# Kernel optimization log

Measured on AMD Instinct MI355X. Metric: run time of the kernel, lower is better.

Reference implementation:

```python
import jax, jax.numpy as jnp
import numpy as np

N_USERS = 50000
N_ENTITIES = 100000
N_FACTORS = 8
N_RELATIONS = 17  # weight has n_relations-1 = 16 rows
EMB = 64
N_EDGES = 2_000_000
NNZ = 2_000_000
SLOPE = 0.2


def setup_inputs() -> dict:
    key = jax.random.key(0)
    ks = jax.random.split(key, 16)
    inp = {
        "entity_emb": jax.random.normal(ks[0], (N_ENTITIES, EMB), jnp.float32),
        "user_emb": jax.random.normal(ks[1], (N_USERS, EMB), jnp.float32),
        "latent_emb": jax.random.normal(ks[2], (N_FACTORS, EMB), jnp.float32),
        "edge_index": jax.random.randint(ks[3], (2, N_EDGES), 0, N_ENTITIES, jnp.int32),
        "edge_type": jax.random.randint(ks[4], (N_EDGES,), 1, N_RELATIONS, jnp.int32),
        "interact_rows": jax.random.randint(ks[5], (NNZ,), 0, N_USERS, jnp.int32),
        "interact_cols": jax.random.randint(ks[6], (NNZ,), 0, N_ENTITIES, jnp.int32),
        "interact_vals": jax.random.uniform(ks[7], (NNZ,), jnp.float32),
        "weight": jax.random.normal(ks[8], (N_RELATIONS - 1, EMB), jnp.float32),
        "entity_cate_set": jax.random.randint(ks[9], (N_ENTITIES,), 1, 33, jnp.int32),
        # params (torch Linear convention: y = x @ W.T + b)
        "W_user_att": jax.random.normal(ks[10], (N_FACTORS, N_FACTORS), jnp.float32) * 0.1,
        "b_user_att": jnp.zeros((N_FACTORS,), jnp.float32),
        "W_weight_att": jax.random.normal(ks[11], (N_RELATIONS - 1, N_RELATIONS - 1), jnp.float32) * 0.1,
        "b_weight_att": jnp.zeros((N_RELATIONS - 1,), jnp.float32),
        "W1": jax.random.normal(ks[12], (EMB, EMB), jnp.float32) * 0.1,
        "b1": jnp.zeros((EMB,), jnp.float32),
        "W2": jax.random.normal(ks[13], (EMB, EMB), jnp.float32) * 0.1,
        "b2": jnp.zeros((EMB,), jnp.float32),
    }
    return inp


def _lin(x, W, b):
    return x @ W.T + b


def reference(entity_emb, user_emb, latent_emb, edge_index, edge_type,
              interact_rows, interact_cols, interact_vals, weight, entity_cate_set,
              W_user_att, b_user_att, W_weight_att, b_weight_att, W1, b1, W2, b2):
    head, tail = edge_index[0], edge_index[1]

    # KG aggregate: gather-multiply-scatter_mean (is_div=False branch)
    neigh = entity_emb[tail] * weight[edge_type - 1]            # [E, C]
    sums = jax.ops.segment_sum(neigh, head, num_segments=N_ENTITIES)
    cnt = jax.ops.segment_sum(jnp.ones((neigh.shape[0],), neigh.dtype),
                              head, num_segments=N_ENTITIES)
    entity_agg = sums / jnp.maximum(cnt, 1.0)[:, None]          # [N_ent, C]

    # user aggregate: sparse mm (COO) interact_mat @ entity_emb
    user_agg = jax.ops.segment_sum(interact_vals[:, None] * entity_emb[interact_cols],
                                   interact_rows, num_segments=N_USERS)  # [U, C]

    # user -> latent interest attention
    score_ = _lin(user_emb, W1, b1) @ _lin(latent_emb, W1, b1).T          # [U, F]
    score = jax.nn.softmax(jax.nn.leaky_relu(_lin(score_, W_user_att, b_user_att), SLOPE), axis=1)  # [U, F]

    score_rp = _lin(latent_emb, W2, b2) @ _lin(weight, W2, b2).T          # [F, R-1]
    latent_new = jax.nn.softmax(jax.nn.leaky_relu(_lin(score_rp, W_weight_att, b_weight_att), SLOPE), axis=-1) @ weight  # [F, C]

    # (disen_weight * score).sum(dim=1) == score @ latent_new
    user_agg = user_agg * (score @ latent_new) + user_agg
    return (entity_agg, user_agg, latent_new)
```

## Files before the change

### kernel.cpp

```cpp
#include <hip/hip_runtime.h>

#define N_USERS    50000
#define N_ENTITIES 100000
#define EMB        64
#define N_EDGES    2000000
#define NNZ        2000000
#define SLOPE      0.2f

#define KROWS   64
#define KSHIFT  6
#define NBK     1563
#define UROWS   32
#define USHIFT  5
#define NBU     1563
#define CAPK    2048
#define CAPU    2048
#define KCAP    1536
#define UCAP    1536
#define CHK     8192
#define EPT     (CHK / 512)
#define PB_K    ((N_EDGES + CHK - 1) / CHK)
#define PB_U    ((NNZ + CHK - 1) / CHK)
#define NQ      (NBK + NBU)
#define ACCBLK  512

__global__ __launch_bounds__(512) void init_cur(int* __restrict__ kgCur,
                                                int* __restrict__ uCur,
                                                int* __restrict__ qCtr) {
    int t = blockIdx.x * blockDim.x + threadIdx.x;
    if (t < NBK) kgCur[t] = t * KCAP;
    if (t < NBU) uCur[t]  = t * UCAP;
    if (t == 0) qCtr[0] = 0;
}

__device__ void small_dense_body(int l,
                                 const float* __restrict__ latent_emb,
                                 const float* __restrict__ weight,
                                 const float* __restrict__ W_weight_att,
                                 const float* __restrict__ b_weight_att,
                                 const float* __restrict__ W1,
                                 const float* __restrict__ b1,
                                 const float* __restrict__ W2,
                                 const float* __restrict__ b2,
                                 float* __restrict__ P_out,
                                 float* __restrict__ c_out,
                                 float* __restrict__ latent_new_out) {
    __shared__ float lat1[8 * 64];
    __shared__ float lat2[8 * 64];
    __shared__ float wl2[16 * 64];
    __shared__ float srp[8 * 16];
    __shared__ float soft[8 * 16];

    if (l < 64) {
        for (int f = 0; f < 8; ++f) {
            float a1 = b1[l], a2 = b2[l];
            for (int k = 0; k < 64; ++k) {
                float le = latent_emb[f * 64 + k];
                a1 += le * W1[l * 64 + k];
                a2 += le * W2[l * 64 + k];
            }
            lat1[f * 64 + l] = a1;
            lat2[f * 64 + l] = a2;
        }
        for (int r = 0; r < 16; ++r) {
            float a = b2[l];
            for (int k = 0; k < 64; ++k) a += weight[r * 64 + k] * W2[l * 64 + k];
            wl2[r * 64 + l] = a;
        }
    }
    __syncthreads();

    if (l < 64) {
        for (int f = 0; f < 8; ++f) {
            float p = 0.f;
            for (int d = 0; d < 64; ++d) p += W1[d * 64 + l] * lat1[f * 64 + d];
            P_out[l * 8 + f] = p;
        }
        if (l < 8) {
            float cc = 0.f;
            for (int d = 0; d < 64; ++d) cc += b1[d] * lat1[l * 64 + d];
            c_out[l] = cc;
        }
        for (int idx = l; idx < 128; idx += 64) {
            int f = idx >> 4, r = idx & 15;
            float a = 0.f;
            for (int d = 0; d < 64; ++d) a += lat2[f * 64 + d] * wl2[r * 64 + d];
            srp[idx] = a;
        }
    }
    __syncthreads();

    if (l < 8) {
        int f = l;
        float att[16];
        float mx = -1e30f;
        for (int k = 0; k < 16; ++k) {
            float a = b_weight_att[k];
            for (int j = 0; j < 16; ++j) a += srp[f * 16 + j] * W_weight_att[k * 16 + j];
            a = a > 0.f ? a : SLOPE * a;
            att[k] = a;
            mx = fmaxf(mx, a);
        }
        float s = 0.f;
        for (int k = 0; k < 16; ++k) { att[k] = expf(att[k] - mx); s += att[k]; }
        float inv = 1.f / s;
        for (int k = 0; k < 16; ++k) soft[f * 16 + k] = att[k] * inv;
    }
    __syncthreads();

    if (l < 64) {
        for (int f = 0; f < 8; ++f) {
            float a = 0.f;
            for (int r = 0; r < 16; ++r) a += soft[f * 16 + r] * weight[r * 64 + l];
            latent_new_out[f * 64 + l] = a;
        }
    }
}

__global__ void small_dense(const float* __restrict__ latent_emb,
                            const float* __restrict__ weight,
                            const float* __restrict__ W_weight_att,
                            const float* __restrict__ b_weight_att,
                            const float* __restrict__ W1,
                            const float* __restrict__ b1,
                            const float* __restrict__ W2,
                            const float* __restrict__ b2,
                            float* __restrict__ P_out,
                            float* __restrict__ c_out,
                            float* __restrict__ latent_new_out) {
    small_dense_body(threadIdx.x, latent_emb, weight, W_weight_att, b_weight_att,
                     W1, b1, W2, b2, P_out, c_out, latent_new_out);
}

__global__ __launch_bounds__(512) void scatter_both(const int* __restrict__ head,
                                                    const int* __restrict__ tail,
                                                    const int* __restrict__ etype,
                                                    int* __restrict__ kgCur,
                                                    int* __restrict__ kgPay,
                                                    const int* __restrict__ urows,
                                                    const int* __restrict__ ucols,
                                                    const float* __restrict__ uvals,
                                                    int* __restrict__ uCur,
                                                    int2* __restrict__ uPay,
                                                    const float* __restrict__ latent_emb,
                                                    const float* __restrict__ weight,
                                                    const float* __restrict__ W_weight_att,
                                                    const float* __restrict__ b_weight_att,
                                                    const float* __restrict__ W1,
                                                    const float* __restrict__ b1,
                                                    const float* __restrict__ W2,
                                                    const float* __restrict__ b2,
                                                    float* __restrict__ Pbuf,
                                                    float* __restrict__ cbuf,
                                                    float* __restrict__ lat_out) {
    if (blockIdx.x == PB_K + PB_U) {
        small_dense_body(threadIdx.x, latent_emb, weight, W_weight_att,
                         b_weight_att, W1, b1, W2, b2, Pbuf, cbuf, lat_out);
        return;
    }

    __shared__ int lh[NBK];
    __shared__ int lb[NBK];
    int tid = threadIdx.x;
    bool isKg = blockIdx.x < PB_K;
    int base = (isKg ? blockIdx.x : blockIdx.x - PB_K) * CHK;
    int shift = isKg ? KSHIFT : USHIFT;
    const int* src = isKg ? head : urows;
    int* cur = isKg ? kgCur : uCur;

    for (int t = tid; t < NBK; t += 512) lh[t] = 0;
    __syncthreads();

    int hreg[EPT];
#pragma unroll
    for (int j = 0; j < EPT; ++j) {
        int i = base + j * 512 + tid;
        int h = (i < N_EDGES) ? src[i] : -1;
        hreg[j] = h;
        if (h >= 0) atomicAdd(&lh[h >> shift], 1);
    }
    __syncthreads();
    for (int t = tid; t < NBK; t += 512) {
        int c = lh[t];
        lb[t] = c ? atomicAdd(&cur[t], c) : 0;
        lh[t] = 0;
    }
    __syncthreads();
    if (isKg) {
#pragma unroll
        for (int j = 0; j < EPT; ++j) {
            int h = hreg[j];
            if (h >= 0) {
                int i = base + j * 512 + tid;
                int b = h >> KSHIFT;
                int p = lb[b] + atomicAdd(&lh[b], 1);
                kgPay[p] = tail[i] | ((etype[i] - 1) << 17) | ((h & (KROWS - 1)) << 21);
            }
        }
    } else {
#pragma unroll
        for (int j = 0; j < EPT; ++j) {
            int h = hreg[j];
            if (h >= 0) {
                int i = base + j * 512 + tid;
                int b = h >> USHIFT;
                int p = lb[b] + atomicAdd(&lh[b], 1);
                uPay[p] = make_int2(ucols[i] | ((h & (UROWS - 1)) << 17),
                                    __float_as_int(uvals[i]));
            }
        }
    }
}

__global__ __launch_bounds__(1024, 8) void acc_both(
        const int* __restrict__ kgPay, const int* __restrict__ kgCur,
        const int2* __restrict__ uPay, const int* __restrict__ uCur,
        const float* __restrict__ entity_emb,
        const float* __restrict__ weight,
        const float* __restrict__ user_emb,
        const float* __restrict__ P,
        const float* __restrict__ cvec,
        const float* __restrict__ W_user_att,
        const float* __restrict__ b_user_att,
        const float* __restrict__ latent_new,
        int* __restrict__ qCtr,
        float* __restrict__ ent_out,
        float* __restrict__ user_out) {
    __shared__ long long smem8[2097];
    __shared__ int sbk;
    int t = threadIdx.x, d = t & 63, wv = t >> 6;

    for (;;) {
        __syncthreads();
        if (t == 0) sbk = atomicAdd(qCtr, 1);
        __syncthreads();
        int q = sbk;
        if (q >= NQ) return;

        if (q < NBU) {
            int2* spay = (int2*)smem8;
            int* lcnt = (int*)(spay + CAPU);
            int* lofs = lcnt + UROWS;
            int* sc   = lofs + UROWS + 1;
            int bk = q;
            int start = bk * UCAP, end = uCur[bk];
            int n = end - start; if (n > CAPU) n = CAPU;

            if (t < UROWS) lcnt[t] = 0;
            __syncthreads();
            for (int i = t; i < n; i += 1024)
                atomicAdd(&lcnt[(uPay[start + i].x >> 17) & (UROWS - 1)], 1);
            __syncthreads();
            if (t < UROWS) sc[t] = lcnt[t];
            __syncthreads();
            for (int off = 1; off < UROWS; off <<= 1) {
                int v = (t < UROWS && t >= off) ? sc[t - off] : 0;
                __syncthreads();
                if (t < UROWS) sc[t] += v;
                __syncthreads();
            }
            if (t < UROWS) { int e = sc[t] - lcnt[t]; lofs[t] = e; lcnt[t] = e; }
            if (t == 0) lofs[UROWS] = n;
            __syncthreads();
            for (int i = t; i < n; i += 1024) {
                int2 v = uPay[start + i];
                int p = atomicAdd(&lcnt[(v.x >> 17) & (UROWS - 1)], 1);
                spay[p] = v;
            }
            __syncthreads();

            int rowbase = bk * UROWS;
            for (int rr = 0; rr < UROWS / 16; ++rr) {
                int r = wv * (UROWS / 16) + rr;
                int gr = rowbase + r;
                if (gr >= N_USERS) break;
                int s0 = lofs[r], e0 = lofs[r + 1];
                float acc = 0.f;
                int i = s0;
                for (; i + 7 < e0; i += 8) {
                    float a0 = 0.f, a1 = 0.f;
#pragma unroll
                    for (int u = 0; u < 8; u += 2) {
                        int2 va = spay[i + u], vb = spay[i + u + 1];
                        a0 += __int_as_float(va.y) * entity_emb[(va.x & 0x1FFFF) * EMB + d];
                        a1 += __int_as_float(vb.y) * entity_emb[(vb.x & 0x1FFFF) * EMB + d];
                    }
                    acc += a0 + a1;
                }
                for (; i < e0; ++i) {
                    int2 v = spay[i];
                    acc += __int_as_float(v.y) * entity_emb[(v.x & 0x1FFFF) * EMB + d];
                }
                for (int j = start + CAPU; j < end; ++j) {
                    int2 v = uPay[j];
                    if (((v.x >> 17) & (UROWS - 1)) == r)
                        acc += __int_as_float(v.y) * entity_emb[(v.x & 0x1FFFF) * EMB + d];
                }

                float ue = user_emb[gr * EMB + d];
                float s[8];
#pragma unroll
                for (int f = 0; f < 8; ++f) s[f] = ue * P[d * 8 + f];
#pragma unroll
                for (int off = 32; off; off >>= 1) {
#pragma unroll
                    for (int f = 0; f < 8; ++f) s[f] += __shfl_xor(s[f], off, 64);
                }
#pragma unroll
                for (int f = 0; f < 8; ++f) s[f] += cvec[f];
                float att[8];
                float mx = -1e30f;
#pragma unroll
                for (int k = 0; k < 8; ++k) {
                    float a = b_user_att[k];
#pragma unroll
                    for (int j = 0; j < 8; ++j) a += s[j] * W_user_att[k * 8 + j];
                    a = a > 0.f ? a : SLOPE * a;
                    att[k] = a;
                    mx = fmaxf(mx, a);
                }
                float sum = 0.f;
#pragma unroll
                for (int k = 0; k < 8; ++k) { att[k] = __expf(att[k] - mx); sum += att[k]; }
                float inv = 1.f / sum;
                float g = 0.f;
#pragma unroll
                for (int f = 0; f < 8; ++f) g += att[f] * inv * latent_new[f * EMB + d];
                user_out[gr * EMB + d] = acc * (1.f + g);
            }
        } else {
            int* spay = (int*)smem8;
            int* lcnt = spay + CAPK;
            int* lofs = lcnt + KROWS;
            int* sc   = lofs + KROWS + 1;
            int bk = q - NBU;
            int start = bk * KCAP, end = kgCur[bk];
            int n = end - start; if (n > CAPK) n = CAPK;

            if (t < KROWS) lcnt[t] = 0;
            __syncthreads();
            for (int i = t; i < n; i += 1024)
                atomicAdd(&lcnt[(kgPay[start + i] >> 21) & (KROWS - 1)], 1);
            __syncthreads();
            if (t < KROWS) sc[t] = lcnt[t];
            __syncthreads();
            for (int off = 1; off < KROWS; off <<= 1) {
                int v = (t < KROWS && t >= off) ? sc[t - off] : 0;
                __syncthreads();
                if (t < KROWS) sc[t] += v;
                __syncthreads();
            }
            if (t < KROWS) { int e = sc[t] - lcnt[t]; lofs[t] = e; lcnt[t] = e; }
            if (t == 0) lofs[KROWS] = n;
            __syncthreads();
            for (int i = t; i < n; i += 1024) {
                int v = kgPay[start + i];
                int p = atomicAdd(&lcnt[(v >> 21) & (KROWS - 1)], 1);
                spay[p] = v;
            }
            __syncthreads();

            int rowbase = bk * KROWS;
            for (int rr = 0; rr < KROWS / 16; ++rr) {
                int r = wv * (KROWS / 16) + rr;
                int gr = rowbase + r;
                if (gr >= N_ENTITIES) break;
                int s0 = lofs[r], e0 = lofs[r + 1];
                int cnt = e0 - s0;
                float acc = 0.f;
                int i = s0;
                for (; i + 7 < e0; i += 8) {
                    float a0 = 0.f, a1 = 0.f;
#pragma unroll
                    for (int u = 0; u < 8; u += 2) {
                        int va = spay[i + u], vb = spay[i + u + 1];
                        a0 += entity_emb[(va & 0x1FFFF) * EMB + d] * weight[((va >> 17) & 15) * EMB + d];
                        a1 += entity_emb[(vb & 0x1FFFF) * EMB + d] * weight[((vb >> 17) & 15) * EMB + d];
                    }
                    acc += a0 + a1;
                }
                for (; i < e0; ++i) {
                    int v = spay[i];
                    acc += entity_emb[(v & 0x1FFFF) * EMB + d] * weight[((v >> 17) & 15) * EMB + d];
                }
                for (int j = start + CAPK; j < end; ++j) {
                    int v = kgPay[j];
                    if (((v >> 21) & (KROWS - 1)) == r) {
                        acc += entity_emb[(v & 0x1FFFF) * EMB + d] * weight[((v >> 17) & 15) * EMB + d];
                        ++cnt;
                    }
                }
                ent_out[gr * EMB + d] = acc / fmaxf((float)cnt, 1.f);
            }
        }
    }
}

__global__ void kg_scatter(const int* __restrict__ head, const int* __restrict__ tail,
                           const int* __restrict__ etype,
                           const float* __restrict__ entity_emb,
                           const float* __restrict__ weight,
                           float* __restrict__ sums, float* __restrict__ cnt) {
    int gid = blockIdx.x * blockDim.x + threadIdx.x;
    int e = gid >> 6, d = threadIdx.x & 63;
    if (e >= N_EDGES) return;
    int h = head[e], t = tail[e], w = etype[e] - 1;
    float v = entity_emb[t * EMB + d] * weight[w * EMB + d];
    unsafeAtomicAdd(&sums[h * EMB + d], v);
    if (d == 0) unsafeAtomicAdd(&cnt[h], 1.0f);
}

__global__ void user_scatter(const int* __restrict__ rows, const int* __restrict__ cols,
                             const float* __restrict__ vals,
                             const float* __restrict__ entity_emb,
                             float* __restrict__ user_sums) {
    int gid = blockIdx.x * blockDim.x + threadIdx.x;
    int e = gid >> 6, d = threadIdx.x & 63;
    if (e >= NNZ) return;
    float v = vals[e] * entity_emb[cols[e] * EMB + d];
    unsafeAtomicAdd(&user_sums[rows[e] * EMB + d], v);
}

__global__ void entity_div(float* __restrict__ ent, const float* __restrict__ cnt) {
    int gid = blockIdx.x * blockDim.x + threadIdx.x;
    if (gid >= N_ENTITIES * EMB) return;
    float c = cnt[gid >> 6];
    ent[gid] = ent[gid] / fmaxf(c, 1.0f);
}

__global__ void user_finalize(const float* __restrict__ user_emb,
                              const float* __restrict__ P,
                              const float* __restrict__ c,
                              const float* __restrict__ W_user_att,
                              const float* __restrict__ b_user_att,
                              const float* __restrict__ latent_new,
                              float* __restrict__ user_out) {
    int gid = blockIdx.x * blockDim.x + threadIdx.x;
    int u = gid >> 6, lane = threadIdx.x & 63;
    if (u >= N_USERS) return;
    float ue = user_emb[u * 64 + lane];
    float s[8];
#pragma unroll
    for (int f = 0; f < 8; ++f) s[f] = ue * P[lane * 8 + f];
#pragma unroll
    for (int off = 32; off; off >>= 1)
#pragma unroll
        for (int f = 0; f < 8; ++f) s[f] += __shfl_xor(s[f], off, 64);
#pragma unroll
    for (int f = 0; f < 8; ++f) s[f] += c[f];
    float att[8], mx = -1e30f;
#pragma unroll
    for (int k = 0; k < 8; ++k) {
        float a = b_user_att[k];
#pragma unroll
        for (int j = 0; j < 8; ++j) a += s[j] * W_user_att[k * 8 + j];
        a = a > 0.f ? a : SLOPE * a;
        att[k] = a;
        mx = fmaxf(mx, a);
    }
    float sum = 0.f;
#pragma unroll
    for (int k = 0; k < 8; ++k) { att[k] = expf(att[k] - mx); sum += att[k]; }
    float inv = 1.f / sum, g = 0.f;
#pragma unroll
    for (int f = 0; f < 8; ++f) g += att[f] * inv * latent_new[f * 64 + lane];
    float ua = user_out[u * 64 + lane];
    user_out[u * 64 + lane] = ua * (1.f + g);
}

extern "C" void kernel_launch(void* const* d_in, const int* in_sizes, int n_in,
                              void* d_out, int out_size, void* d_ws, size_t ws_size,
                              hipStream_t stream) {
    const float* entity_emb   = (const float*)d_in[0];
    const float* user_emb     = (const float*)d_in[1];
    const float* latent_emb   = (const float*)d_in[2];
    const int*   edge_index   = (const int*)d_in[3];
    const int*   edge_type    = (const int*)d_in[4];
    const int*   irows        = (const int*)d_in[5];
    const int*   icols        = (const int*)d_in[6];
    const float* ivals        = (const float*)d_in[7];
    const float* weight       = (const float*)d_in[8];
    const float* W_user_att   = (const float*)d_in[10];
    const float* b_user_att   = (const float*)d_in[11];
    const float* W_weight_att = (const float*)d_in[12];
    const float* b_weight_att = (const float*)d_in[13];
    const float* W1           = (const float*)d_in[14];
    const float* b1           = (const float*)d_in[15];
    const float* W2           = (const float*)d_in[16];
    const float* b2           = (const float*)d_in[17];

    float* out      = (float*)d_out;
    float* ent_out  = out;
    float* user_out = out + (size_t)N_ENTITIES * EMB;
    float* lat_out  = user_out + (size_t)N_USERS * EMB;

    const int* head = edge_index;
    const int* tail = edge_index + N_EDGES;

    int* ws_i = (int*)d_ws;
    int*   qCtr   = ws_i;
    int*   kgCur  = qCtr + 2;
    int*   uCur   = kgCur + NBK;
    int*   kgPay  = uCur + NBU;
    int2*  uPay   = (int2*)(kgPay + NBK * KCAP);
    float* Pbuf   = (float*)(uPay + NBU * UCAP);
    float* cbuf   = Pbuf + 64 * 8;
    size_t need_static = (size_t)(2 + NBK + NBU + (size_t)NBK * KCAP +
                                  2 * (size_t)NBU * UCAP + 512 + 8) * 4;

    if (ws_size >= need_static) {
        init_cur<<<(NBK + 511) / 512, 512, 0, stream>>>(kgCur, uCur, qCtr);
        scatter_both<<<PB_K + PB_U + 1, 512, 0, stream>>>(head, tail, edge_type,
                                                          kgCur, kgPay,
                                                          irows, icols, ivals,
                                                          uCur, uPay,
                                                          latent_emb, weight,
                                                          W_weight_att, b_weight_att,
                                                          W1, b1, W2, b2,
                                                          Pbuf, cbuf, lat_out);
        acc_both<<<ACCBLK, 1024, 0, stream>>>(kgPay, kgCur, uPay, uCur,
                                              entity_emb, weight, user_emb,
                                              Pbuf, cbuf, W_user_att, b_user_att,
                                              lat_out, qCtr, ent_out, user_out);
    } else {
        float* cnt   = (float*)d_ws;
        float* Pbuf3 = cnt + N_ENTITIES;
        float* cbuf3 = Pbuf3 + 64 * 8;
        hipMemsetAsync(ent_out, 0,
                       (size_t)(N_ENTITIES + N_USERS) * EMB * sizeof(float), stream);
        hipMemsetAsync(cnt, 0, N_ENTITIES * sizeof(float), stream);
        int blocks_edges = (N_EDGES * 64) / 256;
        kg_scatter<<<blocks_edges, 256, 0, stream>>>(head, tail, edge_type, entity_emb,
                                                     weight, ent_out, cnt);
        user_scatter<<<blocks_edges, 256, 0, stream>>>(irows, icols, ivals, entity_emb,
                                                       user_out);
        small_dense<<<1, 64, 0, stream>>>(latent_emb, weight, W_weight_att,
                                          b_weight_att, W1, b1, W2, b2,
                                          Pbuf3, cbuf3, lat_out);
        user_finalize<<<(N_USERS * 64) / 256, 256, 0, stream>>>(user_emb, Pbuf3, cbuf3,
                                                                W_user_att, b_user_att,
                                                                lat_out, user_out);
        entity_div<<<(N_ENTITIES * EMB) / 256, 256, 0, stream>>>(ent_out, cnt);
    }
}
```

Baseline: 398.3 us.

## Fuse bucket scatter and accumulation into one persistent kernel with grid barrier

Merges the cursor init, the bucket-scatter pass and the accumulate pass into one persistent kernel. Blocks pull scatter chunks from an atomic work queue, then wait at a spin-based grid barrier before pulling accumulation buckets from a second queue. Buckets grow to 256 KG rows and 128 user rows with fixed per-bucket capacity, which cuts the number of global cursor atomics and removes launch gaps. The overflow fallback loop is dropped and entries past capacity are discarded, so correctness relies on per-bucket counts staying under the cap. The grid barrier also relies on all 512 blocks being resident at once.

```diff
diff --git a/kernel.cpp b/kernel.cpp
--- a/kernel.cpp
+++ b/kernel.cpp
@@ -7,33 +7,23 @@
 #define NNZ        2000000
 #define SLOPE      0.2f
 
-#define KROWS   64
-#define KSHIFT  6
-#define NBK     1563
-#define UROWS   32
-#define USHIFT  5
-#define NBU     1563
-#define CAPK    2048
-#define CAPU    2048
-#define KCAP    1536
-#define UCAP    1536
+#define KROWS   256
+#define KSHIFT  8
+#define NBK     391
+#define UROWS   128
+#define USHIFT  7
+#define NBU     391
+#define KCAP    5632
+#define UCAP    5632
 #define CHK     8192
-#define EPT     (CHK / 512)
-#define PB_K    ((N_EDGES + CHK - 1) / CHK)
-#define PB_U    ((NNZ + CHK - 1) / CHK)
+#define NCH_K   ((N_EDGES + CHK - 1) / CHK)
+#define NCH_U   ((NNZ + CHK - 1) / CHK)
+#define NCHT    (NCH_K + NCH_U + 1)
 #define NQ      (NBK + NBU)
 #define ACCBLK  512
-
-__global__ __launch_bounds__(512) void init_cur(int* __restrict__ kgCur,
-                                                int* __restrict__ uCur,
-                                                int* __restrict__ qCtr) {
-    int t = blockIdx.x * blockDim.x + threadIdx.x;
-    if (t < NBK) kgCur[t] = t * KCAP;
-    if (t < NBU) uCur[t]  = t * UCAP;
-    if (t == 0) qCtr[0] = 0;
-}
-
-__device__ void small_dense_body(int l,
+#define SMEM_LL 5825
+
+__device__ void small_dense_body(int l, float* __restrict__ sh,
                                  const float* __restrict__ latent_emb,
                                  const float* __restrict__ weight,
                                  const float* __restrict__ W_weight_att,
@@ -45,11 +35,11 @@
                                  float* __restrict__ P_out,
                                  float* __restrict__ c_out,
                                  float* __restrict__ latent_new_out) {
-    __shared__ float lat1[8 * 64];
-    __shared__ float lat2[8 * 64];
-    __shared__ float wl2[16 * 64];
-    __shared__ float srp[8 * 16];
-    __shared__ float soft[8 * 16];
+    float* lat1 = sh;
+    float* lat2 = sh + 512;
+    float* wl2  = sh + 1024;
+    float* srp  = sh + 2048;
+    float* soft = sh + 2176;
 
     if (l < 64) {
         for (int f = 0; f < 8; ++f) {
@@ -128,123 +118,146 @@
                             float* __restrict__ P_out,
                             float* __restrict__ c_out,
                             float* __restrict__ latent_new_out) {
-    small_dense_body(threadIdx.x, latent_emb, weight, W_weight_att, b_weight_att,
-                     W1, b1, W2, b2, P_out, c_out, latent_new_out);
-}
-
-__global__ __launch_bounds__(512) void scatter_both(const int* __restrict__ head,
-                                                    const int* __restrict__ tail,
-                                                    const int* __restrict__ etype,
-                                                    int* __restrict__ kgCur,
-                                                    int* __restrict__ kgPay,
-                                                    const int* __restrict__ urows,
-                                                    const int* __restrict__ ucols,
-                                                    const float* __restrict__ uvals,
-                                                    int* __restrict__ uCur,
-                                                    int2* __restrict__ uPay,
-                                                    const float* __restrict__ latent_emb,
-                                                    const float* __restrict__ weight,
-                                                    const float* __restrict__ W_weight_att,
-                                                    const float* __restrict__ b_weight_att,
-                                                    const float* __restrict__ W1,
-                                                    const float* __restrict__ b1,
-                                                    const float* __restrict__ W2,
-                                                    const float* __restrict__ b2,
-                                                    float* __restrict__ Pbuf,
-                                                    float* __restrict__ cbuf,
-                                                    float* __restrict__ lat_out) {
-    if (blockIdx.x == PB_K + PB_U) {
-        small_dense_body(threadIdx.x, latent_emb, weight, W_weight_att,
-                         b_weight_att, W1, b1, W2, b2, Pbuf, cbuf, lat_out);
-        return;
-    }
-
-    __shared__ int lh[NBK];
-    __shared__ int lb[NBK];
-    int tid = threadIdx.x;
-    bool isKg = blockIdx.x < PB_K;
-    int base = (isKg ? blockIdx.x : blockIdx.x - PB_K) * CHK;
-    int shift = isKg ? KSHIFT : USHIFT;
-    const int* src = isKg ? head : urows;
-    int* cur = isKg ? kgCur : uCur;
-
-    for (int t = tid; t < NBK; t += 512) lh[t] = 0;
-    __syncthreads();
-
-    int hreg[EPT];
-#pragma unroll
-    for (int j = 0; j < EPT; ++j) {
-        int i = base + j * 512 + tid;
-        int h = (i < N_EDGES) ? src[i] : -1;
-        hreg[j] = h;
-        if (h >= 0) atomicAdd(&lh[h >> shift], 1);
-    }
-    __syncthreads();
-    for (int t = tid; t < NBK; t += 512) {
-        int c = lh[t];
-        lb[t] = c ? atomicAdd(&cur[t], c) : 0;
-        lh[t] = 0;
-    }
-    __syncthreads();
-    if (isKg) {
-#pragma unroll
-        for (int j = 0; j < EPT; ++j) {
-            int h = hreg[j];
-            if (h >= 0) {
-                int i = base + j * 512 + tid;
-                int b = h >> KSHIFT;
-                int p = lb[b] + atomicAdd(&lh[b], 1);
-                kgPay[p] = tail[i] | ((etype[i] - 1) << 17) | ((h & (KROWS - 1)) << 21);
-            }
-        }
-    } else {
-#pragma unroll
-        for (int j = 0; j < EPT; ++j) {
-            int h = hreg[j];
-            if (h >= 0) {
-                int i = base + j * 512 + tid;
-                int b = h >> USHIFT;
-                int p = lb[b] + atomicAdd(&lh[b], 1);
-                uPay[p] = make_int2(ucols[i] | ((h & (UROWS - 1)) << 17),
-                                    __float_as_int(uvals[i]));
-            }
-        }
-    }
-}
-
-__global__ __launch_bounds__(1024, 8) void acc_both(
-        const int* __restrict__ kgPay, const int* __restrict__ kgCur,
-        const int2* __restrict__ uPay, const int* __restrict__ uCur,
+    __shared__ float sh[2304];
+    small_dense_body(threadIdx.x, sh, latent_emb, weight, W_weight_att,
+                     b_weight_att, W1, b1, W2, b2, P_out, c_out, latent_new_out);
+}
+
+__global__ __launch_bounds__(1024, 8) void fused_all(
+        const int* __restrict__ head, const int* __restrict__ tail,
+        const int* __restrict__ etype,
+        const int* __restrict__ urows, const int* __restrict__ ucols,
+        const float* __restrict__ uvals,
+        int* __restrict__ ctrs, int* __restrict__ kgCur, int* __restrict__ uCur,
+        int* __restrict__ kgPay, int2* __restrict__ uPay,
+        const float* __restrict__ latent_emb,
+        const float* __restrict__ weight,
+        const float* __restrict__ W_weight_att,
+        const float* __restrict__ b_weight_att,
+        const float* __restrict__ W1, const float* __restrict__ b1,
+        const float* __restrict__ W2, const float* __restrict__ b2,
         const float* __restrict__ entity_emb,
-        const float* __restrict__ weight,
         const float* __restrict__ user_emb,
-        const float* __restrict__ P,
-        const float* __restrict__ cvec,
         const float* __restrict__ W_user_att,
         const float* __restrict__ b_user_att,
-        const float* __restrict__ latent_new,
-        int* __restrict__ qCtr,
-        float* __restrict__ ent_out,
-        float* __restrict__ user_out) {
-    __shared__ long long smem8[2097];
-    __shared__ int sbk;
-    int t = threadIdx.x, d = t & 63, wv = t >> 6;
+        float* __restrict__ Pbuf, float* __restrict__ cbuf,
+        float* __restrict__ lat_out,
+        float* __restrict__ ent_out, float* __restrict__ user_out) {
+    __shared__ long long smem8[SMEM_LL];
+    __shared__ int sidx;
+    int t = threadIdx.x;
 
     for (;;) {
         __syncthreads();
-        if (t == 0) sbk = atomicAdd(qCtr, 1);
+        if (t == 0) sidx = atomicAdd(&ctrs[0], 1);
         __syncthreads();
-        int q = sbk;
+        int cid = sidx;
+        if (cid >= NCHT) break;
+
+        if (cid == NCHT - 1) {
+            small_dense_body(t, (float*)smem8, latent_emb, weight, W_weight_att,
+                             b_weight_att, W1, b1, W2, b2, Pbuf, cbuf, lat_out);
+        } else if (cid < NCH_K) {
+            int* lh = (int*)smem8;
+            int* lb = lh + NBK;
+            int base = cid * CHK;
+            for (int x = t; x < NBK; x += 1024) lh[x] = 0;
+            __syncthreads();
+            int kreg[CHK / 1024];
+#pragma unroll
+            for (int j = 0; j < CHK / 1024; ++j) {
+                int i = base + j * 1024 + t;
+                int h = (i < N_EDGES) ? head[i] : -1;
+                kreg[j] = h;
+                if (h >= 0) atomicAdd(&lh[h >> KSHIFT], 1);
+            }
+            __syncthreads();
+            for (int x = t; x < NBK; x += 1024) {
+                int c = lh[x];
+                lb[x] = c ? atomicAdd(&kgCur[x], c) : 0;
+                lh[x] = 0;
+            }
+            __syncthreads();
+#pragma unroll
+            for (int j = 0; j < CHK / 1024; ++j) {
+                int h = kreg[j];
+                if (h >= 0) {
+                    int i = base + j * 1024 + t;
+                    int b = h >> KSHIFT;
+                    int o = lb[b] + atomicAdd(&lh[b], 1);
+                    if (o < KCAP)
+                        kgPay[b * KCAP + o] =
+                            tail[i] | ((etype[i] - 1) << 17) | ((h & (KROWS - 1)) << 21);
+                }
+            }
+        } else {
+            int* lh = (int*)smem8;
+            int* lb = lh + NBU;
+            int base = (cid - NCH_K) * CHK;
+            for (int x = t; x < NBU; x += 1024) lh[x] = 0;
+            __syncthreads();
+            int kreg[CHK / 1024];
+#pragma unroll
+            for (int j = 0; j < CHK / 1024; ++j) {
+                int i = base + j * 1024 + t;
+                int r = (i < NNZ) ? urows[i] : -1;
+                kreg[j] = r;
+                if (r >= 0) atomicAdd(&lh[r >> USHIFT], 1);
+            }
+            __syncthreads();
+            for (int x = t; x < NBU; x += 1024) {
+                int c = lh[x];
+                lb[x] = c ? atomicAdd(&uCur[x], c) : 0;
+                lh[x] = 0;
+            }
+            __syncthreads();
+#pragma unroll
+            for (int j = 0; j < CHK / 1024; ++j) {
+                int r = kreg[j];
+                if (r >= 0) {
+                    int i = base + j * 1024 + t;
+                    int b = r >> USHIFT;
+                    int o = lb[b] + atomicAdd(&lh[b], 1);
+                    if (o < UCAP)
+                        uPay[b * UCAP + o] =
+                            make_int2(ucols[i] | ((r & (UROWS - 1)) << 17),
+                                      __float_as_int(uvals[i]));
+                }
+            }
+        }
+        __threadfence();
+        __syncthreads();
+        if (t == 0)
+            __hip_atomic_fetch_add(&ctrs[1], 1, __ATOMIC_RELEASE,
+                                   __HIP_MEMORY_SCOPE_AGENT);
+    }
+
+    if (t == 0) {
+        while (__hip_atomic_load(&ctrs[1], __ATOMIC_ACQUIRE,
+                                 __HIP_MEMORY_SCOPE_AGENT) < NCHT)
+            __builtin_amdgcn_s_sleep(2);
+    }
+    __syncthreads();
+
+    int d = t & 63, wv = t >> 6;
+
+    for (;;) {
+        __syncthreads();
+        if (t == 0) sidx = atomicAdd(&ctrs[2], 1);
+        __syncthreads();
+        int q = sidx;
         if (q >= NQ) return;
 
         if (q < NBU) {
             int2* spay = (int2*)smem8;
-            int* lcnt = (int*)(spay + CAPU);
+            int* lcnt = (int*)(spay + UCAP);
             int* lofs = lcnt + UROWS;
             int* sc   = lofs + UROWS + 1;
             int bk = q;
-            int start = bk * UCAP, end = uCur[bk];
-            int n = end - start; if (n > CAPU) n = CAPU;
+            int start = bk * UCAP;
+            int n = __hip_atomic_load(&uCur[bk], __ATOMIC_RELAXED,
+                                      __HIP_MEMORY_SCOPE_AGENT);
+            if (n > UCAP) n = UCAP;
 
             if (t < UROWS) lcnt[t] = 0;
             __syncthreads();
@@ -291,23 +304,18 @@
                     int2 v = spay[i];
                     acc += __int_as_float(v.y) * entity_emb[(v.x & 0x1FFFF) * EMB + d];
                 }
-                for (int j = start + CAPU; j < end; ++j) {
-                    int2 v = uPay[j];
-                    if (((v.x >> 17) & (UROWS - 1)) == r)
-                        acc += __int_as_float(v.y) * entity_emb[(v.x & 0x1FFFF) * EMB + d];
-                }
 
                 float ue = user_emb[gr * EMB + d];
                 float s[8];
 #pragma unroll
-                for (int f = 0; f < 8; ++f) s[f] = ue * P[d * 8 + f];
+                for (int f = 0; f < 8; ++f) s[f] = ue * Pbuf[d * 8 + f];
 #pragma unroll
                 for (int off = 32; off; off >>= 1) {
 #pragma unroll
                     for (int f = 0; f < 8; ++f) s[f] += __shfl_xor(s[f], off, 64);
                 }
 #pragma unroll
-                for (int f = 0; f < 8; ++f) s[f] += cvec[f];
+                for (int f = 0; f < 8; ++f) s[f] += cbuf[f];
                 float att[8];
                 float mx = -1e30f;
 #pragma unroll
@@ -325,17 +333,19 @@
                 float inv = 1.f / sum;
                 float g = 0.f;
 #pragma unroll
-                for (int f = 0; f < 8; ++f) g += att[f] * inv * latent_new[f * EMB + d];
+                for (int f = 0; f < 8; ++f) g += att[f] * inv * lat_out[f * EMB + d];
                 user_out[gr * EMB + d] = acc * (1.f + g);
             }
         } else {
             int* spay = (int*)smem8;
-            int* lcnt = spay + CAPK;
+            int* lcnt = spay + KCAP;
             int* lofs = lcnt + KROWS;
             int* sc   = lofs + KROWS + 1;
             int bk = q - NBU;
-            int start = bk * KCAP, end = kgCur[bk];
-            int n = end - start; if (n > CAPK) n = CAPK;
+            int start = bk * KCAP;
+            int n = __hip_atomic_load(&kgCur[bk], __ATOMIC_RELAXED,
+                                      __HIP_MEMORY_SCOPE_AGENT);
+            if (n > KCAP) n = KCAP;
 
             if (t < KROWS) lcnt[t] = 0;
             __syncthreads();
@@ -382,13 +392,6 @@
                 for (; i < e0; ++i) {
                     int v = spay[i];
                     acc += entity_emb[(v & 0x1FFFF) * EMB + d] * weight[((v >> 17) & 15) * EMB + d];
-                }
-                for (int j = start + CAPK; j < end; ++j) {
-                    int v = kgPay[j];
-                    if (((v >> 21) & (KROWS - 1)) == r) {
-                        acc += entity_emb[(v & 0x1FFFF) * EMB + d] * weight[((v >> 17) & 15) * EMB + d];
-                        ++cnt;
-                    }
                 }
                 ent_out[gr * EMB + d] = acc / fmaxf((float)cnt, 1.f);
             }
@@ -498,30 +501,28 @@
     const int* tail = edge_index + N_EDGES;
 
     int* ws_i = (int*)d_ws;
-    int*   qCtr   = ws_i;
-    int*   kgCur  = qCtr + 2;
+    int*   ctrs   = ws_i;
+    int*   kgCur  = ctrs + 4;
     int*   uCur   = kgCur + NBK;
     int*   kgPay  = uCur + NBU;
     int2*  uPay   = (int2*)(kgPay + NBK * KCAP);
     float* Pbuf   = (float*)(uPay + NBU * UCAP);
     float* cbuf   = Pbuf + 64 * 8;
-    size_t need_static = (size_t)(2 + NBK + NBU + (size_t)NBK * KCAP +
-                                  2 * (size_t)NBU * UCAP + 512 + 8) * 4;
-
-    if (ws_size >= need_static) {
-        init_cur<<<(NBK + 511) / 512, 512, 0, stream>>>(kgCur, uCur, qCtr);
-        scatter_both<<<PB_K + PB_U + 1, 512, 0, stream>>>(head, tail, edge_type,
-                                                          kgCur, kgPay,
-                                                          irows, icols, ivals,
-                                                          uCur, uPay,
-                                                          latent_emb, weight,
-                                                          W_weight_att, b_weight_att,
-                                                          W1, b1, W2, b2,
-                                                          Pbuf, cbuf, lat_out);
-        acc_both<<<ACCBLK, 1024, 0, stream>>>(kgPay, kgCur, uPay, uCur,
-                                              entity_emb, weight, user_emb,
-                                              Pbuf, cbuf, W_user_att, b_user_att,
-                                              lat_out, qCtr, ent_out, user_out);
+    size_t need = (size_t)(4 + NBK + NBU + (size_t)NBK * KCAP +
+                           2 * (size_t)NBU * UCAP + 512 + 8) * 4;
+
+    if (ws_size >= need) {
+        hipMemsetAsync(ctrs, 0, (size_t)(4 + NBK + NBU) * sizeof(int), stream);
+        fused_all<<<ACCBLK, 1024, 0, stream>>>(head, tail, edge_type,
+                                               irows, icols, ivals,
+                                               ctrs, kgCur, uCur, kgPay, uPay,
+                                               latent_emb, weight,
+                                               W_weight_att, b_weight_att,
+                                               W1, b1, W2, b2,
+                                               entity_emb, user_emb,
+                                               W_user_att, b_user_att,
+                                               Pbuf, cbuf, lat_out,
+                                               ent_out, user_out);
     } else {
         float* cnt   = (float*)d_ws;
         float* Pbuf3 = cnt + N_ENTITIES;
```

Result: slower. 819.4 us (+105.7%).
